# Optimization experiments

Hardware: AMD Instinct MI355X
Metric: run time of the kernel (lower is better)

Reference implementation:

```python
import jax, jax.numpy as jnp
import numpy as np

N_HEAD = 8

def _l2norm(x, eps=1e-12):
    # F.normalize(p=2, dim=-1): x / max(||x||_2, eps)
    return x / jnp.maximum(jnp.linalg.norm(x, axis=-1, keepdims=True), eps)

def setup_inputs() -> dict:
    key = jax.random.key(0)
    ks = jax.random.split(key, 9)
    B, L, E = 2, 2048, 512
    s = 0.02
    return {
        "query": jax.random.normal(ks[0], (B, L, E), dtype=jnp.float32),
        "Wq": s * jax.random.normal(ks[1], (E, E), dtype=jnp.float32),
        "bq": jnp.zeros((E,), dtype=jnp.float32),
        "Wk": s * jax.random.normal(ks[2], (E, E), dtype=jnp.float32),
        "bk": jnp.zeros((E,), dtype=jnp.float32),
        "Wv": s * jax.random.normal(ks[3], (E, E), dtype=jnp.float32),
        "bv": jnp.zeros((E,), dtype=jnp.float32),
        "Wo": s * jax.random.normal(ks[4], (E, E), dtype=jnp.float32),
        "bo": jnp.zeros((E,), dtype=jnp.float32),
    }

def reference(query, Wq, bq, Wk, bk, Wv, bv, Wo, bo):
    B, L, E = query.shape
    H = N_HEAD
    hd = E // H
    # Faithful to torch: .view(tgt_len, bsz, E) is a RESHAPE, not a transpose.
    x = query.reshape(L, B, E)
    q = jax.nn.relu(x @ Wq.T + bq)
    k = jax.nn.relu(x @ Wk.T + bk)
    v = x @ Wv.T + bv
    q = _l2norm(q)
    k = _l2norm(k)
    # (L, B, E) -> (L, B*H, hd) -> (B*H, L, hd)
    q_ = q.reshape(L, B * H, hd).transpose(1, 0, 2)
    k_ = k.reshape(L, B * H, hd).transpose(1, 0, 2)
    v_ = v.reshape(L, B * H, hd).transpose(1, 0, 2)
    # Causal linear attention: cumulative outer-product of k,v then contract with q.
    kv = jnp.einsum('nld,nlm->nldm', k_, v_)      # [B*H, L, hd, hd]
    kv_cum = jnp.cumsum(kv, axis=1)
    out = jnp.einsum('nld,nldm->nlm', q_, kv_cum)  # [B*H, L, hd]
    out = out.transpose(1, 0, 2).reshape(L, B, E)
    out = out @ Wo.T + bo
    return out.reshape(B, L, E)
```

## Files before the change

### kernel.cpp

```cpp
#include <hip/hip_runtime.h>
#include <hip/hip_bf16.h>

typedef __attribute__((ext_vector_type(8))) short short8;
typedef __attribute__((ext_vector_type(4))) float f32x4;
using bf16 = __hip_bfloat16;

__device__ __forceinline__ unsigned short f2bf(float f) {
    unsigned u = __float_as_uint(f);
    u += 0x7fff + ((u >> 16) & 1);
    return (unsigned short)(u >> 16);
}
__device__ __forceinline__ float bf2f(unsigned short s) {
    return __uint_as_float(((unsigned)s) << 16);
}
__device__ __forceinline__ void gl_lds16(const unsigned short* g, unsigned short* l) {
    __builtin_amdgcn_global_load_lds(
        (const __attribute__((address_space(1))) unsigned int*)g,
        (__attribute__((address_space(3))) unsigned int*)l, 16, 0, 0);
}


__global__ __launch_bounds__(256) void pack_kernel(
    const float* __restrict__ X, const float* __restrict__ Wq, const float* __restrict__ Wk,
    const float* __restrict__ Wv, const float* __restrict__ Wo,
    bf16* __restrict__ Xp, bf16* __restrict__ Wqp, bf16* __restrict__ Wkp,
    bf16* __restrict__ Wvp, bf16* __restrict__ Wop, float* __restrict__ ssq)
{
    __shared__ __align__(16) unsigned short sm[4096];
    int id = blockIdx.x;
    int tid = threadIdx.x;
    if (id < 8) {
        int zi = id * 1024 + tid * 4;
        *(float4*)&ssq[zi] = make_float4(0.f, 0.f, 0.f, 0.f);
    }
    const float* src; unsigned short* dst; int g, sc;
    if (id < 512) { src = X; dst = (unsigned short*)Xp; g = id >> 3; sc = id & 7; }
    else {
        int t = id - 512; int wsel = t >> 6; int u = t & 63;
        g = u >> 3; sc = u & 7;
        src = (wsel == 0) ? Wq : ((wsel == 1) ? Wk : ((wsel == 2) ? Wv : Wo));
        dst = (unsigned short*)((wsel == 0) ? Wqp : ((wsel == 1) ? Wkp : ((wsel == 2) ? Wvp : Wop)));
    }
    int r = tid >> 2, kq = tid & 3;
    const float* sp = src + (size_t)(g * 64 + r) * 512 + sc * 64 + kq * 16;
    #pragma unroll
    for (int i = 0; i < 4; ++i) {
        float4 v = *(const float4*)(sp + i * 4);
        int kk = kq * 16 + i * 4;
        int sl = kk >> 3, el = kk & 7;
        ushort4 u4;
        u4.x = f2bf(v.x); u4.y = f2bf(v.y); u4.z = f2bf(v.z); u4.w = f2bf(v.w);
        *(ushort4*)&sm[(sl * 64 + r) * 8 + el] = u4;
    }
    __syncthreads();
    unsigned short* dp = dst + (size_t)g * 32768 + sc * 4096;
    *(uint4*)(dp + tid * 16)     = *(const uint4*)&sm[tid * 16];
    *(uint4*)(dp + tid * 16 + 8) = *(const uint4*)&sm[tid * 16 + 8];
}

__global__ __launch_bounds__(256) void qkv_gemm_kernel(
    const bf16* __restrict__ Xp,
    const bf16* __restrict__ W0p, const bf16* __restrict__ W1p, const bf16* __restrict__ W2p,
    const float* __restrict__ b0, const float* __restrict__ b1, const float* __restrict__ b2,
    bf16* __restrict__ O0, bf16* __restrict__ O1, bf16* __restrict__ O2,
    float* __restrict__ ssq)
{
    __shared__ __align__(16) unsigned short smem[8192];
    unsigned short* As = smem;
    unsigned short* Bs = smem + 2048;
    int z = blockIdx.z;
    const unsigned short* Wg = (const unsigned short*)((z == 0) ? W0p : ((z == 1) ? W1p : W2p));
    const float* bias = (z == 0) ? b0 : ((z == 1) ? b1 : b2);
    unsigned short* Out = (unsigned short*)((z == 0) ? O0 : ((z == 1) ? O1 : O2));
    const unsigned short* Ag = (const unsigned short*)Xp;

    int g  = blockIdx.x;
    int gB = blockIdx.y * 2;
    int m0 = g * 64;
    int n0 = blockIdx.y * 128;
    int tid = threadIdx.x;
    int lane = tid & 63;
    int w = tid >> 6;
    int wm = (w >> 1) * 32;
    int wn = (w & 1) * 64;
    int fr = lane & 15, qf = lane >> 4;

    f32x4 zero4 = {0.f, 0.f, 0.f, 0.f};
    f32x4 acc[2][4];
    #pragma unroll
    for (int t = 0; t < 2; ++t)
        #pragma unroll
        for (int u = 0; u < 4; ++u) acc[t][u] = zero4;

    for (int kw = 0; kw < 16; ++kw) {
        int s0 = kw * 4;
        __syncthreads();
        gl_lds16(Ag + ((size_t)(g * 64 + s0 + w) * 64 + lane) * 8, As + w * 512);
        gl_lds16(Wg + ((size_t)(gB * 64 + s0 + w) * 64 + lane) * 8, Bs + w * 1024);
        gl_lds16(Wg + ((size_t)((gB + 1) * 64 + s0 + w) * 64 + lane) * 8, Bs + w * 1024 + 512);
        __syncthreads();
        short8 af[2], bfr[4];
        #pragma unroll
        for (int t = 0; t < 2; ++t) af[t] = *(const short8*)&As[(qf * 64 + wm + t * 16 + fr) * 8];
        #pragma unroll
        for (int u = 0; u < 4; ++u) bfr[u] = *(const short8*)&Bs[(qf * 128 + wn + u * 16 + fr) * 8];
        #pragma unroll
        for (int t = 0; t < 2; ++t)
            #pragma unroll
            for (int u = 0; u < 4; ++u)
                acc[t][u] = __builtin_amdgcn_mfma_f32_16x16x32_bf16(af[t], bfr[u], acc[t][u], 0, 0, 0);
    }

    bool relu = (z < 2);
    int rb = qf * 4;
    #pragma unroll
    for (int t = 0; t < 2; ++t)
        #pragma unroll
        for (int u = 0; u < 4; ++u) {
            float bv = bias[n0 + wn + u * 16 + fr];
            #pragma unroll
            for (int r = 0; r < 4; ++r) {
                float v = acc[t][u][r] + bv;
                if (relu) v = fmaxf(v, 0.f);
                acc[t][u][r] = v;
            }
        }
    if (relu) {
        #pragma unroll
        for (int t = 0; t < 2; ++t)
            #pragma unroll
            for (int r = 0; r < 4; ++r) {
                float s = 0.f;
                #pragma unroll
                for (int u = 0; u < 4; ++u) s += acc[t][u][r] * acc[t][u][r];
                #pragma unroll
                for (int off = 1; off < 16; off <<= 1) s += __shfl_xor(s, off, 64);
                if (fr == 0) atomicAdd(&ssq[z * 4096 + m0 + wm + t * 16 + rb + r], s);
            }
    }
    __syncthreads();
    #pragma unroll
    for (int t = 0; t < 2; ++t)
        #pragma unroll
        for (int u = 0; u < 4; ++u)
            #pragma unroll
            for (int r = 0; r < 4; ++r)
                smem[(wm + t * 16 + rb + r) * 128 + wn + u * 16 + fr] = f2bf(acc[t][u][r]);
    __syncthreads();
    #pragma unroll
    for (int rep = 0; rep < 4; ++rep) {
        int idx8 = rep * 256 + tid;
        int row = idx8 >> 4, col8 = (idx8 & 15) * 8;
        *(uint4*)(Out + (size_t)(m0 + row) * 512 + n0 + col8) = *(const uint4*)&smem[row * 128 + col8];
    }
}

__global__ __launch_bounds__(256) void chunk_kv_kernel(
    const bf16* __restrict__ Kb, const bf16* __restrict__ Vb,
    const float* __restrict__ ssq, float* __restrict__ ScT, bf16* __restrict__ Vt_g)
{
    int n = blockIdx.x >> 5, c = blockIdx.x & 31;
    int b = n >> 3, h = n & 7;
    __shared__ float Ks[64 * 64];
    __shared__ float Vs[64 * 64];
    const unsigned short* Kg = (const unsigned short*)Kb;
    const unsigned short* Vg = (const unsigned short*)Vb;
    int tid = threadIdx.x;
    int td = tid >> 4, tm = tid & 15;
    int d0 = td * 4, m0 = tm * 4;
    #pragma unroll
    for (int rep = 0; rep < 4; ++rep) {
        int idx = rep * 1024 + tid * 4;
        int j = idx >> 6, d = idx & 63;
        int grow = (c * 64 + j) * 2 + b;
        ushort4 ku = *(const ushort4*)&Kg[(size_t)grow * 512 + h * 64 + d];
        ushort4 vu = *(const ushort4*)&Vg[(size_t)grow * 512 + h * 64 + d];
        float rk = 1.f / fmaxf(sqrtf(ssq[4096 + grow]), 1e-12f);
        *(float4*)&Ks[j * 64 + d] = make_float4(bf2f(ku.x), bf2f(ku.y), bf2f(ku.z), bf2f(ku.w));
        *(float4*)&Vs[j * 64 + d] = make_float4(bf2f(vu.x) * rk, bf2f(vu.y) * rk,
                                                bf2f(vu.z) * rk, bf2f(vu.w) * rk);
    }
    __syncthreads();
    float acc[4][4] = {};
    for (int j = 0; j < 64; ++j) {
        float4 kv = *(const float4*)&Ks[j * 64 + d0];
        float4 vv = *(const float4*)&Vs[j * 64 + m0];
        acc[0][0] += kv.x*vv.x; acc[0][1] += kv.x*vv.y; acc[0][2] += kv.x*vv.z; acc[0][3] += kv.x*vv.w;
        acc[1][0] += kv.y*vv.x; acc[1][1] += kv.y*vv.y; acc[1][2] += kv.y*vv.z; acc[1][3] += kv.y*vv.w;
        acc[2][0] += kv.z*vv.x; acc[2][1] += kv.z*vv.y; acc[2][2] += kv.z*vv.z; acc[2][3] += kv.z*vv.w;
        acc[3][0] += kv.w*vv.x; acc[3][1] += kv.w*vv.y; acc[3][2] += kv.w*vv.z; acc[3][3] += kv.w*vv.w;
    }
    int vm = tid & 63, vj0 = (tid >> 6) * 16;
    unsigned short tmp[16];
    #pragma unroll
    for (int i = 0; i < 16; ++i) tmp[i] = f2bf(Vs[(vj0 + i) * 64 + vm]);
    size_t vtoff = (size_t)n * 131072 + (size_t)vm * 2048 + c * 64 + vj0;
    *(uint4*)((unsigned short*)Vt_g + vtoff)     = *(uint4*)&tmp[0];
    *(uint4*)((unsigned short*)Vt_g + vtoff + 8) = *(uint4*)&tmp[8];

    float* outp = ScT + (size_t)blockIdx.x * 4096;
    #pragma unroll
    for (int j2 = 0; j2 < 4; ++j2) {
        float4 o4 = make_float4(acc[0][j2], acc[1][j2], acc[2][j2], acc[3][j2]);
        *(float4*)&outp[(m0 + j2) * 64 + d0] = o4;
    }
}

__global__ __launch_bounds__(256) void prefix_kernel(const float* __restrict__ ScT, bf16* __restrict__ SpT)
{
    int n = blockIdx.x >> 4;
    int idx = ((blockIdx.x & 15) << 8) + threadIdx.x;
    size_t base = (size_t)n * 131072 + idx;
    unsigned short* sp = (unsigned short*)SpT;
    float run = 0.f;
    #pragma unroll
    for (int c = 0; c < 32; ++c) {
        size_t off = base + (size_t)c * 4096;
        sp[off] = f2bf(run);
        run += ScT[off];
    }
}

__global__ __launch_bounds__(256) void attn_kernel(
    const bf16* __restrict__ Qb, const bf16* __restrict__ Kb,
    const bf16* __restrict__ Vt_g, const bf16* __restrict__ SpT_g,
    const float* __restrict__ ssq, bf16* __restrict__ AOb)
{
    int n = blockIdx.x >> 5, c = blockIdx.x & 31;
    int b = n >> 3, h = n & 7;
    __shared__ unsigned short Qs[64 * 72];
    __shared__ unsigned short Ks[64 * 72];
    __shared__ unsigned short Vt[64 * 72];
    __shared__ unsigned short Ps[4 * 16 * 40];
    int tid = threadIdx.x;
    int lane = tid & 63;
    int w = tid >> 6;
    int fr = lane & 15, q = lane >> 4;

    const unsigned short* Qg = (const unsigned short*)Qb;
    const unsigned short* Kg = (const unsigned short*)Kb;
    const unsigned short* Vg = (const unsigned short*)Vt_g;

    #pragma unroll
    for (int rep = 0; rep < 2; ++rep) {
        int idx = rep * 256 + tid;
        int l = idx >> 3, dc = (idx & 7) * 8;
        size_t goff = (size_t)((c * 64 + l) * 2 + b) * 512 + h * 64 + dc;
        *(uint4*)&Qs[l * 72 + dc] = *(const uint4*)(Qg + goff);
        *(uint4*)&Ks[l * 72 + dc] = *(const uint4*)(Kg + goff);
        int m = l, jc = dc;
        *(uint4*)&Vt[m * 72 + jc] =
            *(const uint4*)(Vg + (size_t)n * 131072 + (size_t)m * 2048 + c * 64 + jc);
    }
    __syncthreads();

    short8 qf[2];
    #pragma unroll
    for (int kh = 0; kh < 2; ++kh)
        qf[kh] = *(const short8*)&Qs[(w * 16 + fr) * 72 + kh * 32 + q * 8];

    f32x4 zero4 = {0.f, 0.f, 0.f, 0.f};
    f32x4 oacc[4];
    #pragma unroll
    for (int mt = 0; mt < 4; ++mt) oacc[mt] = zero4;

    const unsigned short* spg = (const unsigned short*)SpT_g + (size_t)blockIdx.x * 4096;
    #pragma unroll
    for (int mt = 0; mt < 4; ++mt) {
        #pragma unroll
        for (int kh = 0; kh < 2; ++kh) {
            short8 sf = *(const short8*)&spg[(mt * 16 + fr) * 64 + kh * 32 + q * 8];
            oacc[mt] = __builtin_amdgcn_mfma_f32_16x16x32_bf16(qf[kh], sf, oacc[mt], 0, 0, 0);
        }
    }

    unsigned short* myPs = &Ps[w * 640];
    int rbase = q * 4;
    int njt = (w >> 1) + 1;
    for (int jt = 0; jt < njt; ++jt) {
        f32x4 pacc[2];
        pacc[0] = zero4; pacc[1] = zero4;
        #pragma unroll
        for (int jt16 = 0; jt16 < 2; ++jt16) {
            #pragma unroll
            for (int kh = 0; kh < 2; ++kh) {
                short8 kf = *(const short8*)&Ks[(jt * 32 + jt16 * 16 + fr) * 72 + kh * 32 + q * 8];
                pacc[jt16] = __builtin_amdgcn_mfma_f32_16x16x32_bf16(qf[kh], kf, pacc[jt16], 0, 0, 0);
            }
        }
        bool diag = (jt == njt - 1);
        int lloc = w * 16 + rbase;
        #pragma unroll
        for (int jt16 = 0; jt16 < 2; ++jt16)
            #pragma unroll
            for (int r = 0; r < 4; ++r) {
                int jl = jt * 32 + jt16 * 16 + fr;
                float pv = pacc[jt16][r];
                if (diag && jl > lloc + r) pv = 0.f;
                myPs[(rbase + r) * 40 + jt16 * 16 + fr] = f2bf(pv);
            }
        short8 pf = *(const short8*)&myPs[fr * 40 + q * 8];
        #pragma unroll
        for (int mt = 0; mt < 4; ++mt) {
            short8 vf = *(const short8*)&Vt[(mt * 16 + fr) * 72 + jt * 32 + q * 8];
            oacc[mt] = __builtin_amdgcn_mfma_f32_16x16x32_bf16(pf, vf, oacc[mt], 0, 0, 0);
        }
    }

    float rqv[4];
    #pragma unroll
    for (int r = 0; r < 4; ++r) {
        int flat = (c * 64 + w * 16 + rbase + r) * 2 + b;
        rqv[r] = 1.f / fmaxf(sqrtf(ssq[flat]), 1e-12f);
    }
    __syncthreads();
    #pragma unroll
    for (int mt = 0; mt < 4; ++mt)
        #pragma unroll
        for (int r = 0; r < 4; ++r)
            Qs[(w * 16 + rbase + r) * 64 + mt * 16 + fr] = f2bf(oacc[mt][r] * rqv[r]);
    __syncthreads();
    #pragma unroll
    for (int rep = 0; rep < 2; ++rep) {
        int idx8 = rep * 256 + tid;
        int l = idx8 >> 3, m8 = (idx8 & 7) * 8;
        *(uint4*)((unsigned short*)AOb + (size_t)((c * 64 + l) * 2 + b) * 512 + h * 64 + m8) =
            *(const uint4*)&Qs[l * 64 + m8];
    }
}

__global__ __launch_bounds__(256) void oproj_kernel(
    const bf16* __restrict__ A, const bf16* __restrict__ Wop,
    const float* __restrict__ bias, float* __restrict__ Out)
{
    __shared__ __align__(16) unsigned short smem[8192];
    unsigned short* As = smem;
    unsigned short* Bs = smem + 2560;
    const unsigned short* Ag = (const unsigned short*)A;
    const unsigned short* Wg = (const unsigned short*)Wop;
    int m0 = blockIdx.x * 64;
    int gy = blockIdx.y;
    int n0 = gy * 64;
    int tid = threadIdx.x;
    int lane = tid & 63;
    int w = tid >> 6;
    int fr = lane & 15, qf = lane >> 4;
    int wm = (w >> 1) * 32;
    int wn = (w & 1) * 32;
    int srow = tid >> 2;
    int skk  = (tid & 3) * 8;

    f32x4 zero4 = {0.f, 0.f, 0.f, 0.f};
    f32x4 acc[2][2];
    acc[0][0] = zero4; acc[0][1] = zero4; acc[1][0] = zero4; acc[1][1] = zero4;

    for (int kw = 0; kw < 16; ++kw) {
        int k0 = kw * 32, s0 = kw * 4;
        __syncthreads();
        *(uint4*)&As[srow * 40 + skk] = *(const uint4*)(Ag + (size_t)(m0 + srow) * 512 + k0 + skk);
        gl_lds16(Wg + ((size_t)(gy * 64 + s0 + w) * 64 + lane) * 8, Bs + w * 512);
        __syncthreads();
        short8 af[2], bf[2];
        #pragma unroll
        for (int t = 0; t < 2; ++t) af[t] = *(const short8*)&As[(wm + t * 16 + fr) * 40 + qf * 8];
        #pragma unroll
        for (int u = 0; u < 2; ++u) bf[u] = *(const short8*)&Bs[(qf * 64 + wn + u * 16 + fr) * 8];
        #pragma unroll
        for (int t = 0; t < 2; ++t)
            #pragma unroll
            for (int u = 0; u < 2; ++u)
                acc[t][u] = __builtin_amdgcn_mfma_f32_16x16x32_bf16(af[t], bf[u], acc[t][u], 0, 0, 0);
    }

    int rb = qf * 4;
    float* Cf = (float*)smem;
    __syncthreads();
    #pragma unroll
    for (int t = 0; t < 2; ++t)
        #pragma unroll
        for (int u = 0; u < 2; ++u) {
            float bv = bias[n0 + wn + u * 16 + fr];
            #pragma unroll
            for (int r = 0; r < 4; ++r)
                Cf[(wm + t * 16 + rb + r) * 64 + wn + u * 16 + fr] = acc[t][u][r] + bv;
        }
    __syncthreads();
    #pragma unroll
    for (int rep = 0; rep < 4; ++rep) {
        int idx = rep * 256 + tid;
        int row = idx >> 4, c4 = (idx & 15) * 4;
        *(float4*)(Out + (size_t)(m0 + row) * 512 + n0 + c4) = *(const float4*)&Cf[row * 64 + c4];
    }
}

extern "C" void kernel_launch(void* const* d_in, const int* in_sizes, int n_in,
                              void* d_out, int out_size, void* d_ws, size_t ws_size,
                              hipStream_t stream)
{
    (void)in_sizes; (void)n_in; (void)out_size; (void)ws_size;
    const float* x  = (const float*)d_in[0];
    const float* Wq = (const float*)d_in[1];
    const float* bq = (const float*)d_in[2];
    const float* Wk = (const float*)d_in[3];
    const float* bk = (const float*)d_in[4];
    const float* Wv = (const float*)d_in[5];
    const float* bv = (const float*)d_in[6];
    const float* Wo = (const float*)d_in[7];
    const float* bo = (const float*)d_in[8];
    float* out = (float*)d_out;

    float* ssq = (float*)d_ws;
    bf16* Xp  = (bf16*)(ssq + 8192);
    bf16* Wqp = Xp + 2097152;
    bf16* Wkp = Wqp + 262144;
    bf16* Wvp = Wkp + 262144;
    bf16* Wop = Wvp + 262144;
    bf16* Qb  = Wop + 262144;
    bf16* Kb  = Qb + 2097152;
    bf16* Vb  = Kb + 2097152;
    bf16* Vt  = Vb + 2097152;
    bf16* AOb = Vt + 2097152;
    bf16* SpT = AOb + 2097152;
    float* ScT = (float*)(SpT + 2097152);

    pack_kernel<<<768, 256, 0, stream>>>(x, Wq, Wk, Wv, Wo, Xp, Wqp, Wkp, Wvp, Wop, ssq);
    qkv_gemm_kernel<<<dim3(64, 4, 3), 256, 0, stream>>>(Xp, Wqp, Wkp, Wvp, bq, bk, bv, Qb, Kb, Vb, ssq);
    chunk_kv_kernel<<<dim3(512), 256, 0, stream>>>(Kb, Vb, ssq, ScT, Vt);
    prefix_kernel<<<dim3(256), 256, 0, stream>>>(ScT, SpT);
    attn_kernel<<<dim3(512), 256, 0, stream>>>(Qb, Kb, Vt, SpT, ssq, AOb);
    oproj_kernel<<<dim3(64, 8), 256, 0, stream>>>(AOb, Wop, bo, out);
}
```

Baseline: 122.7 us.

## Fuse chunk-kv, prefix, attention and output projection into one flag-synchronized kernel

Replaces four separate launches (chunk kv-state, prefix scan, intra-chunk attention, output projection) with a single persistent-style kernel of 512 blocks. Blocks signal per-chunk completion through global atomic flags, and each block sums the preceding chunk states itself instead of relying on a separate prefix kernel. The output-projection phase waits on a per-chunk counter before reading the attention output. This removes launch gaps and the SpT round trip, but it relies on all 512 blocks being co-resident for the spin-waits to make progress. It also adds redundant O(c) prefix summation per block.

New measurement: 411.1 us. 3.35x slower.

```diff
diff --git a/kernel.cpp b/kernel.cpp
--- a/kernel.cpp
+++ b/kernel.cpp
@@ -18,13 +18,23 @@
         (const __attribute__((address_space(1))) unsigned int*)g,
         (__attribute__((address_space(3))) unsigned int*)l, 16, 0, 0);
 }
+__device__ __forceinline__ int aload(const int* p) {
+    return __hip_atomic_load(p, __ATOMIC_ACQUIRE, __HIP_MEMORY_SCOPE_AGENT);
+}
+__device__ __forceinline__ void astore(int* p, int v) {
+    __hip_atomic_store(p, v, __ATOMIC_RELEASE, __HIP_MEMORY_SCOPE_AGENT);
+}
+__device__ __forceinline__ void aadd(int* p, int v) {
+    __hip_atomic_fetch_add(p, v, __ATOMIC_RELEASE, __HIP_MEMORY_SCOPE_AGENT);
+}
 
 
 __global__ __launch_bounds__(256) void pack_kernel(
     const float* __restrict__ X, const float* __restrict__ Wq, const float* __restrict__ Wk,
     const float* __restrict__ Wv, const float* __restrict__ Wo,
     bf16* __restrict__ Xp, bf16* __restrict__ Wqp, bf16* __restrict__ Wkp,
-    bf16* __restrict__ Wvp, bf16* __restrict__ Wop, float* __restrict__ ssq)
+    bf16* __restrict__ Wvp, bf16* __restrict__ Wop, float* __restrict__ ssq,
+    int* __restrict__ flg)
 {
     __shared__ __align__(16) unsigned short sm[4096];
     int id = blockIdx.x;
@@ -32,6 +42,8 @@
     if (id < 8) {
         int zi = id * 1024 + tid * 4;
         *(float4*)&ssq[zi] = make_float4(0.f, 0.f, 0.f, 0.f);
+    } else if (id == 8) {
+        *(int4*)&flg[tid * 4] = make_int4(0, 0, 0, 0);
     }
     const float* src; unsigned short* dst; int g, sc;
     if (id < 512) { src = X; dst = (unsigned short*)Xp; g = id >> 3; sc = id & 7; }
@@ -155,241 +167,253 @@
     }
 }
 
-__global__ __launch_bounds__(256) void chunk_kv_kernel(
-    const bf16* __restrict__ Kb, const bf16* __restrict__ Vb,
-    const float* __restrict__ ssq, float* __restrict__ ScT, bf16* __restrict__ Vt_g)
+__global__ __launch_bounds__(256) void tail_kernel(
+    const bf16* __restrict__ Qb, const bf16* __restrict__ Kb, const bf16* __restrict__ Vb,
+    bf16* __restrict__ Vt_g, bf16* __restrict__ AOb,
+    float* __restrict__ ScT, const float* __restrict__ ssq, int* __restrict__ flg,
+    const bf16* __restrict__ Wop, const float* __restrict__ bo, float* __restrict__ out)
 {
-    int n = blockIdx.x >> 5, c = blockIdx.x & 31;
-    int b = n >> 3, h = n & 7;
-    __shared__ float Ks[64 * 64];
-    __shared__ float Vs[64 * 64];
-    const unsigned short* Kg = (const unsigned short*)Kb;
-    const unsigned short* Vg = (const unsigned short*)Vb;
-    int tid = threadIdx.x;
-    int td = tid >> 4, tm = tid & 15;
-    int d0 = td * 4, m0 = tm * 4;
-    #pragma unroll
-    for (int rep = 0; rep < 4; ++rep) {
-        int idx = rep * 1024 + tid * 4;
-        int j = idx >> 6, d = idx & 63;
-        int grow = (c * 64 + j) * 2 + b;
-        ushort4 ku = *(const ushort4*)&Kg[(size_t)grow * 512 + h * 64 + d];
-        ushort4 vu = *(const ushort4*)&Vg[(size_t)grow * 512 + h * 64 + d];
-        float rk = 1.f / fmaxf(sqrtf(ssq[4096 + grow]), 1e-12f);
-        *(float4*)&Ks[j * 64 + d] = make_float4(bf2f(ku.x), bf2f(ku.y), bf2f(ku.z), bf2f(ku.w));
-        *(float4*)&Vs[j * 64 + d] = make_float4(bf2f(vu.x) * rk, bf2f(vu.y) * rk,
-                                                bf2f(vu.z) * rk, bf2f(vu.w) * rk);
-    }
-    __syncthreads();
-    float acc[4][4] = {};
-    for (int j = 0; j < 64; ++j) {
-        float4 kv = *(const float4*)&Ks[j * 64 + d0];
-        float4 vv = *(const float4*)&Vs[j * 64 + m0];
-        acc[0][0] += kv.x*vv.x; acc[0][1] += kv.x*vv.y; acc[0][2] += kv.x*vv.z; acc[0][3] += kv.x*vv.w;
-        acc[1][0] += kv.y*vv.x; acc[1][1] += kv.y*vv.y; acc[1][2] += kv.y*vv.z; acc[1][3] += kv.y*vv.w;
-        acc[2][0] += kv.z*vv.x; acc[2][1] += kv.z*vv.y; acc[2][2] += kv.z*vv.z; acc[2][3] += kv.z*vv.w;
-        acc[3][0] += kv.w*vv.x; acc[3][1] += kv.w*vv.y; acc[3][2] += kv.w*vv.z; acc[3][3] += kv.w*vv.w;
-    }
-    int vm = tid & 63, vj0 = (tid >> 6) * 16;
-    unsigned short tmp[16];
-    #pragma unroll
-    for (int i = 0; i < 16; ++i) tmp[i] = f2bf(Vs[(vj0 + i) * 64 + vm]);
-    size_t vtoff = (size_t)n * 131072 + (size_t)vm * 2048 + c * 64 + vj0;
-    *(uint4*)((unsigned short*)Vt_g + vtoff)     = *(uint4*)&tmp[0];
-    *(uint4*)((unsigned short*)Vt_g + vtoff + 8) = *(uint4*)&tmp[8];
-
-    float* outp = ScT + (size_t)blockIdx.x * 4096;
-    #pragma unroll
-    for (int j2 = 0; j2 < 4; ++j2) {
-        float4 o4 = make_float4(acc[0][j2], acc[1][j2], acc[2][j2], acc[3][j2]);
-        *(float4*)&outp[(m0 + j2) * 64 + d0] = o4;
-    }
-}
-
-__global__ __launch_bounds__(256) void prefix_kernel(const float* __restrict__ ScT, bf16* __restrict__ SpT)
-{
-    int n = blockIdx.x >> 4;
-    int idx = ((blockIdx.x & 15) << 8) + threadIdx.x;
-    size_t base = (size_t)n * 131072 + idx;
-    unsigned short* sp = (unsigned short*)SpT;
-    float run = 0.f;
-    #pragma unroll
-    for (int c = 0; c < 32; ++c) {
-        size_t off = base + (size_t)c * 4096;
-        sp[off] = f2bf(run);
-        run += ScT[off];
-    }
-}
-
-__global__ __launch_bounds__(256) void attn_kernel(
-    const bf16* __restrict__ Qb, const bf16* __restrict__ Kb,
-    const bf16* __restrict__ Vt_g, const bf16* __restrict__ SpT_g,
-    const float* __restrict__ ssq, bf16* __restrict__ AOb)
-{
-    int n = blockIdx.x >> 5, c = blockIdx.x & 31;
-    int b = n >> 3, h = n & 7;
-    __shared__ unsigned short Qs[64 * 72];
-    __shared__ unsigned short Ks[64 * 72];
-    __shared__ unsigned short Vt[64 * 72];
-    __shared__ unsigned short Ps[4 * 16 * 40];
+    __shared__ __align__(16) unsigned char SMraw[43008];
+    int blk = blockIdx.x;
     int tid = threadIdx.x;
     int lane = tid & 63;
     int w = tid >> 6;
     int fr = lane & 15, q = lane >> 4;
-
-    const unsigned short* Qg = (const unsigned short*)Qb;
-    const unsigned short* Kg = (const unsigned short*)Kb;
-    const unsigned short* Vg = (const unsigned short*)Vt_g;
-
-    #pragma unroll
-    for (int rep = 0; rep < 2; ++rep) {
-        int idx = rep * 256 + tid;
-        int l = idx >> 3, dc = (idx & 7) * 8;
-        size_t goff = (size_t)((c * 64 + l) * 2 + b) * 512 + h * 64 + dc;
-        *(uint4*)&Qs[l * 72 + dc] = *(const uint4*)(Qg + goff);
-        *(uint4*)&Ks[l * 72 + dc] = *(const uint4*)(Kg + goff);
-        int m = l, jc = dc;
-        *(uint4*)&Vt[m * 72 + jc] =
-            *(const uint4*)(Vg + (size_t)n * 131072 + (size_t)m * 2048 + c * 64 + jc);
-    }
-    __syncthreads();
-
-    short8 qf[2];
-    #pragma unroll
-    for (int kh = 0; kh < 2; ++kh)
-        qf[kh] = *(const short8*)&Qs[(w * 16 + fr) * 72 + kh * 32 + q * 8];
-
     f32x4 zero4 = {0.f, 0.f, 0.f, 0.f};
-    f32x4 oacc[4];
-    #pragma unroll
-    for (int mt = 0; mt < 4; ++mt) oacc[mt] = zero4;
-
-    const unsigned short* spg = (const unsigned short*)SpT_g + (size_t)blockIdx.x * 4096;
-    #pragma unroll
-    for (int mt = 0; mt < 4; ++mt) {
-        #pragma unroll
-        for (int kh = 0; kh < 2; ++kh) {
-            short8 sf = *(const short8*)&spg[(mt * 16 + fr) * 64 + kh * 32 + q * 8];
-            oacc[mt] = __builtin_amdgcn_mfma_f32_16x16x32_bf16(qf[kh], sf, oacc[mt], 0, 0, 0);
-        }
-    }
-
-    unsigned short* myPs = &Ps[w * 640];
-    int rbase = q * 4;
-    int njt = (w >> 1) + 1;
-    for (int jt = 0; jt < njt; ++jt) {
-        f32x4 pacc[2];
-        pacc[0] = zero4; pacc[1] = zero4;
-        #pragma unroll
-        for (int jt16 = 0; jt16 < 2; ++jt16) {
+    int n = blk >> 5, c = blk & 31;
+    int b = n >> 3, h = n & 7;
+
+    {
+        float* Ksf = (float*)SMraw;
+        float* Vsf = Ksf + 4096;
+        const unsigned short* Kg = (const unsigned short*)Kb;
+        const unsigned short* Vg = (const unsigned short*)Vb;
+        int td = tid >> 4, tm = tid & 15;
+        int d0 = td * 4, m0 = tm * 4;
+        #pragma unroll
+        for (int rep = 0; rep < 4; ++rep) {
+            int idx = rep * 1024 + tid * 4;
+            int j = idx >> 6, d = idx & 63;
+            int grow = (c * 64 + j) * 2 + b;
+            ushort4 ku = *(const ushort4*)&Kg[(size_t)grow * 512 + h * 64 + d];
+            ushort4 vu = *(const ushort4*)&Vg[(size_t)grow * 512 + h * 64 + d];
+            float rk = 1.f / fmaxf(sqrtf(ssq[4096 + grow]), 1e-12f);
+            *(float4*)&Ksf[j * 64 + d] = make_float4(bf2f(ku.x), bf2f(ku.y), bf2f(ku.z), bf2f(ku.w));
+            *(float4*)&Vsf[j * 64 + d] = make_float4(bf2f(vu.x) * rk, bf2f(vu.y) * rk,
+                                                     bf2f(vu.z) * rk, bf2f(vu.w) * rk);
+        }
+        __syncthreads();
+        float acc[4][4] = {};
+        for (int j = 0; j < 64; ++j) {
+            float4 kv = *(const float4*)&Ksf[j * 64 + d0];
+            float4 vv = *(const float4*)&Vsf[j * 64 + m0];
+            acc[0][0] += kv.x*vv.x; acc[0][1] += kv.x*vv.y; acc[0][2] += kv.x*vv.z; acc[0][3] += kv.x*vv.w;
+            acc[1][0] += kv.y*vv.x; acc[1][1] += kv.y*vv.y; acc[1][2] += kv.y*vv.z; acc[1][3] += kv.y*vv.w;
+            acc[2][0] += kv.z*vv.x; acc[2][1] += kv.z*vv.y; acc[2][2] += kv.z*vv.z; acc[2][3] += kv.z*vv.w;
+            acc[3][0] += kv.w*vv.x; acc[3][1] += kv.w*vv.y; acc[3][2] += kv.w*vv.z; acc[3][3] += kv.w*vv.w;
+        }
+        int vm = tid & 63, vj0 = (tid >> 6) * 16;
+        unsigned short tmp[16];
+        #pragma unroll
+        for (int i = 0; i < 16; ++i) tmp[i] = f2bf(Vsf[(vj0 + i) * 64 + vm]);
+        size_t vtoff = (size_t)n * 131072 + (size_t)vm * 2048 + c * 64 + vj0;
+        *(uint4*)((unsigned short*)Vt_g + vtoff)     = *(uint4*)&tmp[0];
+        *(uint4*)((unsigned short*)Vt_g + vtoff + 8) = *(uint4*)&tmp[8];
+
+        float* outp = ScT + (size_t)blk * 4096;
+        #pragma unroll
+        for (int j2 = 0; j2 < 4; ++j2) {
+            float4 o4 = make_float4(acc[0][j2], acc[1][j2], acc[2][j2], acc[3][j2]);
+            *(float4*)&outp[(m0 + j2) * 64 + d0] = o4;
+        }
+        __threadfence();
+        __syncthreads();
+        if (tid == 0) astore(&flg[blk], 1);
+    }
+
+    unsigned short* Sps = (unsigned short*)SMraw;
+    {
+        if (c > 0 && tid < c)
+            while (aload(&flg[n * 32 + tid]) == 0) __builtin_amdgcn_s_sleep(1);
+        __syncthreads();
+        __threadfence();
+        const float* scb = ScT + (size_t)(n * 32) * 4096;
+        float4 a4[4];
+        #pragma unroll
+        for (int s = 0; s < 4; ++s) a4[s] = make_float4(0.f, 0.f, 0.f, 0.f);
+        for (int cp = 0; cp < c; ++cp) {
+            #pragma unroll
+            for (int s = 0; s < 4; ++s) {
+                float4 v = *(const float4*)&scb[(size_t)cp * 4096 + s * 1024 + tid * 4];
+                a4[s].x += v.x; a4[s].y += v.y; a4[s].z += v.z; a4[s].w += v.w;
+            }
+        }
+        __syncthreads();
+        #pragma unroll
+        for (int s = 0; s < 4; ++s) {
+            int E = s * 1024 + tid * 4;
+            int m = E >> 6, d = E & 63;
+            ushort4 u4;
+            u4.x = f2bf(a4[s].x); u4.y = f2bf(a4[s].y); u4.z = f2bf(a4[s].z); u4.w = f2bf(a4[s].w);
+            *(ushort4*)&Sps[m * 72 + d] = u4;
+        }
+    }
+
+    {
+        unsigned short* Qs = (unsigned short*)(SMraw + 9216);
+        unsigned short* Ks = (unsigned short*)(SMraw + 18432);
+        unsigned short* Vt = (unsigned short*)(SMraw + 27648);
+        unsigned short* Ps = (unsigned short*)(SMraw + 36864);
+        const unsigned short* Qg = (const unsigned short*)Qb;
+        const unsigned short* Kg = (const unsigned short*)Kb;
+        const unsigned short* Vg = (const unsigned short*)Vt_g;
+
+        #pragma unroll
+        for (int rep = 0; rep < 2; ++rep) {
+            int idx = rep * 256 + tid;
+            int l = idx >> 3, dc = (idx & 7) * 8;
+            size_t goff = (size_t)((c * 64 + l) * 2 + b) * 512 + h * 64 + dc;
+            *(uint4*)&Qs[l * 72 + dc] = *(const uint4*)(Qg + goff);
+            *(uint4*)&Ks[l * 72 + dc] = *(const uint4*)(Kg + goff);
+            *(uint4*)&Vt[l * 72 + dc] =
+                *(const uint4*)(Vg + (size_t)n * 131072 + (size_t)l * 2048 + c * 64 + dc);
+        }
+        __syncthreads();
+
+        short8 qfv[2];
+        #pragma unroll
+        for (int kh = 0; kh < 2; ++kh)
+            qfv[kh] = *(const short8*)&Qs[(w * 16 + fr) * 72 + kh * 32 + q * 8];
+
+        f32x4 oacc[4];
+        #pragma unroll
+        for (int mt = 0; mt < 4; ++mt) oacc[mt] = zero4;
+
+        #pragma unroll
+        for (int mt = 0; mt < 4; ++mt) {
             #pragma unroll
             for (int kh = 0; kh < 2; ++kh) {
-                short8 kf = *(const short8*)&Ks[(jt * 32 + jt16 * 16 + fr) * 72 + kh * 32 + q * 8];
-                pacc[jt16] = __builtin_amdgcn_mfma_f32_16x16x32_bf16(qf[kh], kf, pacc[jt16], 0, 0, 0);
-            }
-        }
-        bool diag = (jt == njt - 1);
-        int lloc = w * 16 + rbase;
-        #pragma unroll
-        for (int jt16 = 0; jt16 < 2; ++jt16)
-            #pragma unroll
-            for (int r = 0; r < 4; ++r) {
-                int jl = jt * 32 + jt16 * 16 + fr;
-                float pv = pacc[jt16][r];
-                if (diag && jl > lloc + r) pv = 0.f;
-                myPs[(rbase + r) * 40 + jt16 * 16 + fr] = f2bf(pv);
-            }
-        short8 pf = *(const short8*)&myPs[fr * 40 + q * 8];
-        #pragma unroll
-        for (int mt = 0; mt < 4; ++mt) {
-            short8 vf = *(const short8*)&Vt[(mt * 16 + fr) * 72 + jt * 32 + q * 8];
-            oacc[mt] = __builtin_amdgcn_mfma_f32_16x16x32_bf16(pf, vf, oacc[mt], 0, 0, 0);
-        }
-    }
-
-    float rqv[4];
-    #pragma unroll
-    for (int r = 0; r < 4; ++r) {
-        int flat = (c * 64 + w * 16 + rbase + r) * 2 + b;
-        rqv[r] = 1.f / fmaxf(sqrtf(ssq[flat]), 1e-12f);
-    }
-    __syncthreads();
-    #pragma unroll
-    for (int mt = 0; mt < 4; ++mt)
-        #pragma unroll
-        for (int r = 0; r < 4; ++r)
-            Qs[(w * 16 + rbase + r) * 64 + mt * 16 + fr] = f2bf(oacc[mt][r] * rqv[r]);
-    __syncthreads();
-    #pragma unroll
-    for (int rep = 0; rep < 2; ++rep) {
-        int idx8 = rep * 256 + tid;
-        int l = idx8 >> 3, m8 = (idx8 & 7) * 8;
-        *(uint4*)((unsigned short*)AOb + (size_t)((c * 64 + l) * 2 + b) * 512 + h * 64 + m8) =
-            *(const uint4*)&Qs[l * 64 + m8];
-    }
-}
-
-__global__ __launch_bounds__(256) void oproj_kernel(
-    const bf16* __restrict__ A, const bf16* __restrict__ Wop,
-    const float* __restrict__ bias, float* __restrict__ Out)
-{
-    __shared__ __align__(16) unsigned short smem[8192];
-    unsigned short* As = smem;
-    unsigned short* Bs = smem + 2560;
-    const unsigned short* Ag = (const unsigned short*)A;
-    const unsigned short* Wg = (const unsigned short*)Wop;
-    int m0 = blockIdx.x * 64;
-    int gy = blockIdx.y;
-    int n0 = gy * 64;
-    int tid = threadIdx.x;
-    int lane = tid & 63;
-    int w = tid >> 6;
-    int fr = lane & 15, qf = lane >> 4;
-    int wm = (w >> 1) * 32;
-    int wn = (w & 1) * 32;
-    int srow = tid >> 2;
-    int skk  = (tid & 3) * 8;
-
-    f32x4 zero4 = {0.f, 0.f, 0.f, 0.f};
-    f32x4 acc[2][2];
-    acc[0][0] = zero4; acc[0][1] = zero4; acc[1][0] = zero4; acc[1][1] = zero4;
-
-    for (int kw = 0; kw < 16; ++kw) {
-        int k0 = kw * 32, s0 = kw * 4;
-        __syncthreads();
-        *(uint4*)&As[srow * 40 + skk] = *(const uint4*)(Ag + (size_t)(m0 + srow) * 512 + k0 + skk);
-        gl_lds16(Wg + ((size_t)(gy * 64 + s0 + w) * 64 + lane) * 8, Bs + w * 512);
-        __syncthreads();
-        short8 af[2], bf[2];
-        #pragma unroll
-        for (int t = 0; t < 2; ++t) af[t] = *(const short8*)&As[(wm + t * 16 + fr) * 40 + qf * 8];
-        #pragma unroll
-        for (int u = 0; u < 2; ++u) bf[u] = *(const short8*)&Bs[(qf * 64 + wn + u * 16 + fr) * 8];
+                short8 sf = *(const short8*)&Sps[(mt * 16 + fr) * 72 + kh * 32 + q * 8];
+                oacc[mt] = __builtin_amdgcn_mfma_f32_16x16x32_bf16(qfv[kh], sf, oacc[mt], 0, 0, 0);
+            }
+        }
+
+        unsigned short* myPs = &Ps[w * 640];
+        int rbase = q * 4;
+        int njt = (w >> 1) + 1;
+        for (int jt = 0; jt < njt; ++jt) {
+            f32x4 pacc[2];
+            pacc[0] = zero4; pacc[1] = zero4;
+            #pragma unroll
+            for (int jt16 = 0; jt16 < 2; ++jt16) {
+                #pragma unroll
+                for (int kh = 0; kh < 2; ++kh) {
+                    short8 kf = *(const short8*)&Ks[(jt * 32 + jt16 * 16 + fr) * 72 + kh * 32 + q * 8];
+                    pacc[jt16] = __builtin_amdgcn_mfma_f32_16x16x32_bf16(qfv[kh], kf, pacc[jt16], 0, 0, 0);
+                }
+            }
+            bool diag = (jt == njt - 1);
+            int lloc = w * 16 + rbase;
+            #pragma unroll
+            for (int jt16 = 0; jt16 < 2; ++jt16)
+                #pragma unroll
+                for (int r = 0; r < 4; ++r) {
+                    int jl = jt * 32 + jt16 * 16 + fr;
+                    float pv = pacc[jt16][r];
+                    if (diag && jl > lloc + r) pv = 0.f;
+                    myPs[(rbase + r) * 40 + jt16 * 16 + fr] = f2bf(pv);
+                }
+            short8 pf = *(const short8*)&myPs[fr * 40 + q * 8];
+            #pragma unroll
+            for (int mt = 0; mt < 4; ++mt) {
+                short8 vf = *(const short8*)&Vt[(mt * 16 + fr) * 72 + jt * 32 + q * 8];
+                oacc[mt] = __builtin_amdgcn_mfma_f32_16x16x32_bf16(pf, vf, oacc[mt], 0, 0, 0);
+            }
+        }
+
+        float rqv[4];
+        #pragma unroll
+        for (int r = 0; r < 4; ++r) {
+            int flat = (c * 64 + w * 16 + rbase + r) * 2 + b;
+            rqv[r] = 1.f / fmaxf(sqrtf(ssq[flat]), 1e-12f);
+        }
+        __syncthreads();
+        #pragma unroll
+        for (int mt = 0; mt < 4; ++mt)
+            #pragma unroll
+            for (int r = 0; r < 4; ++r)
+                Qs[(w * 16 + rbase + r) * 64 + mt * 16 + fr] = f2bf(oacc[mt][r] * rqv[r]);
+        __syncthreads();
+        #pragma unroll
+        for (int rep = 0; rep < 2; ++rep) {
+            int idx8 = rep * 256 + tid;
+            int l = idx8 >> 3, m8 = (idx8 & 7) * 8;
+            *(uint4*)((unsigned short*)AOb + (size_t)((c * 64 + l) * 2 + b) * 512 + h * 64 + m8) =
+                *(const uint4*)&Qs[l * 64 + m8];
+        }
+        __threadfence();
+        __syncthreads();
+        if (tid == 0) aadd(&flg[512 + c], 1);
+    }
+
+    {
+        int x = blk & 63, y = blk >> 6;
+        int m0 = x * 64, n0 = y * 64;
+        int cneed = x >> 1;
+        if (tid == 0)
+            while (aload(&flg[512 + cneed]) < 16) __builtin_amdgcn_s_sleep(1);
+        __syncthreads();
+        __threadfence();
+
+        unsigned short* As = (unsigned short*)SMraw;
+        unsigned short* Bs = (unsigned short*)(SMraw + 5120);
+        const unsigned short* Ag = (const unsigned short*)AOb;
+        const unsigned short* Wg = (const unsigned short*)Wop;
+        int wm = (w >> 1) * 32;
+        int wn = (w & 1) * 32;
+        int srow = tid >> 2;
+        int skk  = (tid & 3) * 8;
+
+        f32x4 acc[2][2];
+        acc[0][0] = zero4; acc[0][1] = zero4; acc[1][0] = zero4; acc[1][1] = zero4;
+
+        for (int kw = 0; kw < 16; ++kw) {
+            int k0 = kw * 32, s0 = kw * 4;
+            __syncthreads();
+            *(uint4*)&As[srow * 40 + skk] = *(const uint4*)(Ag + (size_t)(m0 + srow) * 512 + k0 + skk);
+            gl_lds16(Wg + ((size_t)(y * 64 + s0 + w) * 64 + lane) * 8, Bs + w * 512);
+            __syncthreads();
+            short8 af[2], bf[2];
+            #pragma unroll
+            for (int t = 0; t < 2; ++t) af[t] = *(const short8*)&As[(wm + t * 16 + fr) * 40 + q * 8];
+            #pragma unroll
+            for (int u = 0; u < 2; ++u) bf[u] = *(const short8*)&Bs[(q * 64 + wn + u * 16 + fr) * 8];
+            #pragma unroll
+            for (int t = 0; t < 2; ++t)
+                #pragma unroll
+                for (int u = 0; u < 2; ++u)
+                    acc[t][u] = __builtin_amdgcn_mfma_f32_16x16x32_bf16(af[t], bf[u], acc[t][u], 0, 0, 0);
+        }
+
+        int rb = q * 4;
+        float* Cf = (float*)SMraw;
+        __syncthreads();
         #pragma unroll
         for (int t = 0; t < 2; ++t)
             #pragma unroll
-            for (int u = 0; u < 2; ++u)
-                acc[t][u] = __builtin_amdgcn_mfma_f32_16x16x32_bf16(af[t], bf[u], acc[t][u], 0, 0, 0);
-    }
-
-    int rb = qf * 4;
-    float* Cf = (float*)smem;
-    __syncthreads();
-    #pragma unroll
-    for (int t = 0; t < 2; ++t)
-        #pragma unroll
-        for (int u = 0; u < 2; ++u) {
-            float bv = bias[n0 + wn + u * 16 + fr];
-            #pragma unroll
-            for (int r = 0; r < 4; ++r)
-                Cf[(wm + t * 16 + rb + r) * 64 + wn + u * 16 + fr] = acc[t][u][r] + bv;
-        }
-    __syncthreads();
-    #pragma unroll
-    for (int rep = 0; rep < 4; ++rep) {
-        int idx = rep * 256 + tid;
-        int row = idx >> 4, c4 = (idx & 15) * 4;
-        *(float4*)(Out + (size_t)(m0 + row) * 512 + n0 + c4) = *(const float4*)&Cf[row * 64 + c4];
+            for (int u = 0; u < 2; ++u) {
+                float bv = bo[n0 + wn + u * 16 + fr];
+                #pragma unroll
+                for (int r = 0; r < 4; ++r)
+                    Cf[(wm + t * 16 + rb + r) * 64 + wn + u * 16 + fr] = acc[t][u][r] + bv;
+            }
+        __syncthreads();
+        #pragma unroll
+        for (int rep = 0; rep < 4; ++rep) {
+            int idx = rep * 256 + tid;
+            int row = idx >> 4, c4 = (idx & 15) * 4;
+            *(float4*)(out + (size_t)(m0 + row) * 512 + n0 + c4) = *(const float4*)&Cf[row * 64 + c4];
+        }
     }
 }
 
@@ -410,7 +434,8 @@
     float* out = (float*)d_out;
 
     float* ssq = (float*)d_ws;
-    bf16* Xp  = (bf16*)(ssq + 8192);
+    int* flg = (int*)(ssq + 8192);
+    bf16* Xp  = (bf16*)(flg + 1024);
     bf16* Wqp = Xp + 2097152;
     bf16* Wkp = Wqp + 262144;
     bf16* Wvp = Wkp + 262144;
@@ -420,13 +445,9 @@
     bf16* Vb  = Kb + 2097152;
     bf16* Vt  = Vb + 2097152;
     bf16* AOb = Vt + 2097152;
-    bf16* SpT = AOb + 2097152;
-    float* ScT = (float*)(SpT + 2097152);
-
-    pack_kernel<<<768, 256, 0, stream>>>(x, Wq, Wk, Wv, Wo, Xp, Wqp, Wkp, Wvp, Wop, ssq);
+    float* ScT = (float*)(AOb + 2097152);
+
+    pack_kernel<<<768, 256, 0, stream>>>(x, Wq, Wk, Wv, Wo, Xp, Wqp, Wkp, Wvp, Wop, ssq, flg);
     qkv_gemm_kernel<<<dim3(64, 4, 3), 256, 0, stream>>>(Xp, Wqp, Wkp, Wvp, bq, bk, bv, Qb, Kb, Vb, ssq);
-    chunk_kv_kernel<<<dim3(512), 256, 0, stream>>>(Kb, Vb, ssq, ScT, Vt);
-    prefix_kernel<<<dim3(256), 256, 0, stream>>>(ScT, SpT);
-    attn_kernel<<<dim3(512), 256, 0, stream>>>(Qb, Kb, Vt, SpT, ssq, AOb);
-    oproj_kernel<<<dim3(64, 8), 256, 0, stream>>>(AOb, Wop, bo, out);
-}
+    tail_kernel<<<512, 256, 0, stream>>>(Qb, Kb, Vb, Vt, AOb, ScT, ssq, flg, Wop, bo, out);
+}
```
